# Kernel optimization log

Measured on AMD Instinct MI355X. Metric: run time of the kernel, lower is better.

## Reference

```python
import jax, jax.numpy as jnp
import numpy as np

DIM = 192
NUM_HEADS = 6
WH, WW = 7, 7
N = WH * WW  # 49 tokens per window
C2 = 2 * DIM  # concatenated channel dim = 384
SCALE = (DIM // NUM_HEADS) ** -0.5  # module uses dim//num_heads, not C2//num_heads
NW = 64  # number of windows per image
B_ = 2048  # num_windows * batch


def _relative_position_index():
    ch = np.arange(WH)
    cw = np.arange(WW)
    coords = np.stack(np.meshgrid(ch, cw, indexing='ij')).reshape(2, -1)  # [2, N]
    rel = coords[:, :, None] - coords[:, None, :]  # [2, N, N]
    rel = rel.transpose(1, 2, 0).astype(np.int64)  # [N, N, 2]
    rel[..., 0] += WH - 1
    rel[..., 1] += WW - 1
    rel[..., 0] *= 2 * WW - 1
    return jnp.asarray(rel.sum(-1))  # [N, N]

REL_IDX = _relative_position_index()


def setup_inputs() -> dict:
    key = jax.random.key(0)
    ks = jax.random.split(key, 8)
    x = jax.random.normal(ks[0], (B_, N, DIM), dtype=jnp.float32)
    y = jax.random.normal(ks[1], (B_, N, DIM), dtype=jnp.float32)
    mask = jax.random.normal(ks[2], (NW, N, N), dtype=jnp.float32)
    w_qkv = jax.random.normal(ks[3], (6 * DIM, C2), dtype=jnp.float32) * 0.02
    b_qkv = jnp.zeros((6 * DIM,), dtype=jnp.float32)
    w_proj = jax.random.normal(ks[4], (DIM, C2), dtype=jnp.float32) * 0.02
    b_proj = jnp.zeros((DIM,), dtype=jnp.float32)
    bias_table = jax.random.normal(ks[5], ((2 * WH - 1) * (2 * WW - 1), NUM_HEADS), dtype=jnp.float32) * 0.02
    return {"x": x, "y": y, "mask": mask, "w_qkv": w_qkv, "b_qkv": b_qkv,
            "w_proj": w_proj, "b_proj": b_proj, "bias_table": bias_table}


def reference(x, y, mask, w_qkv, b_qkv, w_proj, b_proj, bias_table):
    Bc = x.shape[0]
    Dh = C2 // NUM_HEADS  # 64
    xy = jnp.concatenate([x, y], axis=2)  # [B_, N, 2*dim]
    qkv = xy @ w_qkv.T + b_qkv  # [B_, N, 6*dim]
    qkv = qkv.reshape(Bc, N, 3, NUM_HEADS, Dh).transpose(2, 0, 3, 1, 4)  # [3, B_, H, N, Dh]
    q, k, v = qkv[0] * SCALE, qkv[1], qkv[2]
    attn = jnp.einsum('bhnd,bhmd->bhnm', q, k)  # [B_, H, N, N]
    rpb = bias_table[REL_IDX]  # [N, N, H]
    attn = attn + rpb.transpose(2, 0, 1)[None]
    nW = mask.shape[0]
    attn = attn.reshape(Bc // nW, nW, NUM_HEADS, N, N) + mask[None, :, None]
    attn = attn.reshape(Bc, NUM_HEADS, N, N)
    attn = jax.nn.softmax(attn, axis=-1)
    out = jnp.einsum('bhnm,bhmd->bhnd', attn, v)  # [B_, H, N, Dh]
    out = out.transpose(0, 2, 1, 3).reshape(Bc, N, C2)
    return out @ w_proj.T + b_proj  # [B_, N, dim]
```

## Files before the change

kernel.cpp:

```cpp
#include <hip/hip_runtime.h>
#include <hip/hip_bf16.h>


typedef __attribute__((ext_vector_type(8))) short short8;
typedef __attribute__((ext_vector_type(4))) float f32x4;

#define SCALE 0.17677669529663687f

#define WQF_OFF    0ul
#define WQF_BYTES  (864ul*1024)
#define WPF_OFF    (WQF_OFF + WQF_BYTES)
#define WPF_BYTES  (144ul*1024)
#define COMB_OFF   (WPF_OFF + WPF_BYTES)
#define COMB_BYTES (64ul*6*4096*4)
#define WS_NEED    (COMB_OFF + COMB_BYTES)

__device__ __forceinline__ unsigned short f2bf(float f){
  unsigned u = __builtin_bit_cast(unsigned, f);
  u = u + 0x7fffu + ((u >> 16) & 1u);
  return (unsigned short)(u >> 16);
}
__device__ __forceinline__ unsigned long long pack4(float4 v){
  return (unsigned long long)f2bf(v.x) | ((unsigned long long)f2bf(v.y) << 16)
       | ((unsigned long long)f2bf(v.z) << 32) | ((unsigned long long)f2bf(v.w) << 48);
}

__device__ __forceinline__ unsigned short cvt1(float x){
  unsigned r;
  asm("v_cvt_pk_bf16_f32 %0, %1, %1" : "=v"(r) : "v"(x));
  return (unsigned short)r;
}
__device__ __forceinline__ uint2 pk4(float a, float b, float c, float d){
  unsigned lo, hi;
  asm("v_cvt_pk_bf16_f32 %0, %1, %2" : "=v"(lo) : "v"(a), "v"(b));
  asm("v_cvt_pk_bf16_f32 %0, %1, %2" : "=v"(hi) : "v"(c), "v"(d));
  return make_uint2(lo, hi);
}

__global__ void k0_wfrag(const float* __restrict__ wq_f, const float* __restrict__ wp_f,
                         unsigned short* __restrict__ wqf, unsigned short* __restrict__ wpf){
  int t = blockIdx.x*256 + threadIdx.x;
  int fragidx = t >> 6, l = t & 63;
  const float* src; unsigned short* dst;
  float sc = 1.0f;
  if (fragidx < 864){
    int h = fragidx/144, rem = fragidx - h*144;
    int ct = rem/12, kt = rem - ct*12;
    int row = (ct>>2)*384 + h*64 + (ct&3)*16 + (l&15);
    src = wq_f + (long)row*384 + kt*32 + (l>>4)*8;
    dst = wqf + (long)fragidx*512 + l*8;
    if (ct < 4) sc = SCALE;
  } else {
    int fid = fragidx - 864;
    int ct = fid/12, kt = fid - ct*12;
    int row = ct*16 + (l&15);
    src = wp_f + (long)row*384 + kt*32 + (l>>4)*8;
    dst = wpf + (long)fid*512 + l*8;
  }
  short8 v;
  #pragma unroll
  for (int e = 0; e < 8; ++e) v[e] = (short)f2bf(src[e] * sc);
  *(short8*)dst = v;
}

__global__ void prep_comb(const float* __restrict__ mask, const float* __restrict__ btab,
                          float* __restrict__ comb){
  int idx = blockIdx.x * 256 + threadIdx.x;
  int j = idx & 63, i = (idx >> 6) & 63, rest = idx >> 12;
  int h = rest % 6, w = rest / 6;
  float v;
  if (i < 49 && j < 49){
    int di = i / 7 - j / 7 + 6;
    int dj = i % 7 - j % 7 + 6;
    v = btab[(di * 13 + dj) * 6 + h] + mask[(w * 49 + i) * 49 + j];
  } else {
    v = (j >= 49) ? -1e30f : 0.0f;
  }
  comb[idx] = v;
}

__device__ __forceinline__ int swz(int r, int b){ return b ^ ((r & 7) << 4); }
__device__ __forceinline__ int a_q (int r, int c){ return 49152 + swz(r, r*128 + c*2); }
__device__ __forceinline__ int a_k (int r, int c){ return 57344 + swz(r, r*128 + c*2); }
__device__ __forceinline__ int a_vt(int r, int c){ return 65536 + swz(r, r*128 + c*2); }
#define OBUF 73728

__global__ __launch_bounds__(256, 2)
void k_fused(const float* __restrict__ x, const float* __restrict__ y,
             const unsigned short* __restrict__ wqf, const unsigned short* __restrict__ wpf,
             const float* __restrict__ bqkv, const float* __restrict__ bproj,
             const float* __restrict__ comb, float* __restrict__ out){
  __shared__ __align__(16) unsigned char smem[81920];
  const int win = blockIdx.x;
  const int tid = threadIdx.x, w = tid>>6, l = tid&63, l15 = l&15, lg = l>>4;

  #pragma unroll
  for (int i = 0; i < 12; ++i){
    int f  = w*12 + i;
    int kt = f >> 2, mt = f & 3;
    int row = mt*16 + l15;
    int c   = kt*32 + lg*8;
    uint4 vv = make_uint4(0,0,0,0);
    if (row < 49){
      const float* src = (c < 192) ? (x + ((long)win*49 + row)*192 + c)
                                   : (y + ((long)win*49 + row)*192 + (c - 192));
      float4 f0 = *(const float4*)src, f1 = *(const float4*)(src + 4);
      uint2 lo = pk4(f0.x, f0.y, f0.z, f0.w);
      uint2 hi = pk4(f1.x, f1.y, f1.z, f1.w);
      vv = make_uint4(lo.x, lo.y, hi.x, hi.y);
    }
    *(uint4*)(smem + f*1024 + l*16) = vv;
  }

  int np[3];
  f32x4 pacc[4][3];
  #pragma unroll
  for (int nt = 0; nt < 3; ++nt){
    np[nt] = w*48 + nt*16 + l15;
    float bv = bproj[np[nt]];
    #pragma unroll
    for (int mt = 0; mt < 4; ++mt)
      #pragma unroll
      for (int j = 0; j < 4; ++j) pacc[mt][nt][j] = bv;
  }

  __syncthreads();

  #pragma unroll 1
  for (int h = 0; h < 6; ++h){
    const float* cb = comb + ((long)((win & 63)*6 + h))*4096 + (w*16 + l15)*64 + lg*4;
    float4 cbv[4];
    #pragma unroll
    for (int nt = 0; nt < 4; ++nt) cbv[nt] = *(const float4*)(cb + nt*16);

    float bias[3];
    #pragma unroll
    for (int nt = 0; nt < 3; ++nt){
      int ct = w*3 + nt, s = ct >> 2;
      bias[nt] = bqkv[s*384 + h*64 + (ct & 3)*16 + l15];
      if (s == 0) bias[nt] *= SCALE;
    }

    const unsigned short* Bb = wqf + ((long)h*12 + w*3)*12*512;
    short8 bB[2][3];
    #pragma unroll
    for (int nt = 0; nt < 3; ++nt)
      bB[0][nt] = *(const short8*)(Bb + (nt*12)*512 + l*8);
    f32x4 acc[4][3];
    #pragma unroll
    for (int mt = 0; mt < 4; ++mt)
      #pragma unroll
      for (int nt = 0; nt < 3; ++nt)
        #pragma unroll
        for (int j = 0; j < 4; ++j) acc[mt][nt][j] = bias[nt];

    #pragma unroll
    for (int kt = 0; kt < 12; ++kt){
      const int cur = kt & 1, nxt = cur ^ 1;
      if (kt < 11){
        #pragma unroll
        for (int nt = 0; nt < 3; ++nt)
          bB[nxt][nt] = *(const short8*)(Bb + (nt*12 + kt+1)*512 + l*8);
      }
      short8 aA[4];
      #pragma unroll
      for (int mt = 0; mt < 4; ++mt)
        aA[mt] = *(const short8*)(smem + (kt*4 + mt)*1024 + l*16);
      __builtin_amdgcn_s_setprio(1);
      #pragma unroll
      for (int nt = 0; nt < 3; ++nt){
        #pragma unroll
        for (int mt = 0; mt < 4; ++mt)
          acc[mt][nt] = __builtin_amdgcn_mfma_f32_16x16x32_bf16(aA[mt], bB[cur][nt], acc[mt][nt], 0, 0, 0);
      }
      __builtin_amdgcn_s_setprio(0);
    }

    #pragma unroll
    for (int nt = 0; nt < 3; ++nt){
      int ct = w*3 + nt, s = ct >> 2, d16 = (ct & 3) * 16;
      if (s == 2){
        #pragma unroll
        for (int mt = 0; mt < 4; ++mt){
          uint2 p = pk4(acc[mt][nt][0], acc[mt][nt][1], acc[mt][nt][2], acc[mt][nt][3]);
          *(uint2*)(smem + a_vt(d16 + l15, mt*16 + lg*4)) = p;
        }
      } else {
        #pragma unroll
        for (int mt = 0; mt < 4; ++mt){
          #pragma unroll
          for (int j = 0; j < 4; ++j){
            int row = mt*16 + lg*4 + j;
            int addr = (s == 0) ? a_q(row, d16 + l15) : a_k(row, d16 + l15);
            *(unsigned short*)(smem + addr) = cvt1(acc[mt][nt][j]);
          }
        }
      }
    }
    __syncthreads();

    short8 bq[2];
    #pragma unroll
    for (int ks = 0; ks < 2; ++ks)
      bq[ks] = *(const short8*)(smem + a_q(w*16 + l15, ks*32 + lg*8));
    f32x4 st[4] = {};
    __builtin_amdgcn_s_setprio(1);
    #pragma unroll
    for (int ks = 0; ks < 2; ++ks){
      #pragma unroll
      for (int nt = 0; nt < 4; ++nt){
        short8 ak = *(const short8*)(smem + a_k(nt*16 + l15, ks*32 + lg*8));
        st[nt] = __builtin_amdgcn_mfma_f32_16x16x32_bf16(ak, bq[ks], st[nt], 0, 0, 0);
      }
    }
    __builtin_amdgcn_s_setprio(0);
    #pragma unroll
    for (int nt = 0; nt < 4; ++nt){
      st[nt][0] += cbv[nt].x; st[nt][1] += cbv[nt].y;
      st[nt][2] += cbv[nt].z; st[nt][3] += cbv[nt].w;
    }
    float mx;
    {
      float m0 = fmaxf(fmaxf(st[0][0], st[0][1]), fmaxf(st[0][2], st[0][3]));
      float m1 = fmaxf(fmaxf(st[1][0], st[1][1]), fmaxf(st[1][2], st[1][3]));
      float m2 = fmaxf(fmaxf(st[2][0], st[2][1]), fmaxf(st[2][2], st[2][3]));
      float m3 = fmaxf(fmaxf(st[3][0], st[3][1]), fmaxf(st[3][2], st[3][3]));
      mx = fmaxf(fmaxf(m0, m1), fmaxf(m2, m3));
    }
    mx = fmaxf(mx, __shfl_xor(mx, 16));
    mx = fmaxf(mx, __shfl_xor(mx, 32));
    float ssum = 0.f;
    #pragma unroll
    for (int nt = 0; nt < 4; ++nt){
      #pragma unroll
      for (int j = 0; j < 4; ++j){
        float e = __expf(st[nt][j] - mx);
        st[nt][j] = e; ssum += e;
      }
    }
    ssum += __shfl_xor(ssum, 16);
    ssum += __shfl_xor(ssum, 32);
    const float inv = 1.0f / ssum;

    #pragma unroll
    for (int nt = 0; nt < 4; ++nt){
      uint2 p = pk4(st[nt][0]*inv, st[nt][1]*inv, st[nt][2]*inv, st[nt][3]*inv);
      *(uint2*)(smem + a_q(w*16 + l15, nt*16 + lg*4)) = p;
    }

    short8 ap[2];
    #pragma unroll
    for (int ks = 0; ks < 2; ++ks)
      ap[ks] = *(const short8*)(smem + a_q(w*16 + l15, ks*32 + lg*8));
    f32x4 oacc[4] = {};
    __builtin_amdgcn_s_setprio(1);
    #pragma unroll
    for (int ks = 0; ks < 2; ++ks){
      #pragma unroll
      for (int nt = 0; nt < 4; ++nt){
        short8 bv = *(const short8*)(smem + a_vt(nt*16 + l15, ks*32 + lg*8));
        oacc[nt] = __builtin_amdgcn_mfma_f32_16x16x32_bf16(ap[ks], bv, oacc[nt], 0, 0, 0);
      }
    }
    __builtin_amdgcn_s_setprio(0);
    #pragma unroll
    for (int nt = 0; nt < 4; ++nt){
      int frag  = (nt >> 1)*4 + w;
      int chunk0 = (lg*4) + ((nt & 1)*2 + (l15 >> 3))*16;
      #pragma unroll
      for (int j = 0; j < 4; ++j){
        int addr = OBUF + frag*1024 + (chunk0 + j)*16 + (l15 & 7)*2;
        *(unsigned short*)(smem + addr) = cvt1(oacc[nt][j]);
      }
    }
    __syncthreads();

    #pragma unroll
    for (int ks = 0; ks < 2; ++ks){
      short8 aO[4];
      #pragma unroll
      for (int mt = 0; mt < 4; ++mt)
        aO[mt] = *(const short8*)(smem + OBUF + (ks*4 + mt)*1024 + l*16);
      __builtin_amdgcn_s_setprio(1);
      #pragma unroll
      for (int nt = 0; nt < 3; ++nt){
        short8 bb = *(const short8*)(wpf + ((long)(w*3 + nt)*12 + h*2 + ks)*512 + l*8);
        #pragma unroll
        for (int mt = 0; mt < 4; ++mt)
          pacc[mt][nt] = __builtin_amdgcn_mfma_f32_16x16x32_bf16(aO[mt], bb, pacc[mt][nt], 0, 0, 0);
      }
      __builtin_amdgcn_s_setprio(0);
    }
  }

  #pragma unroll
  for (int mt = 0; mt < 4; ++mt){
    #pragma unroll
    for (int j = 0; j < 4; ++j){
      int row = mt*16 + lg*4 + j;
      if (row < 49){
        float* o = out + ((long)win*49 + row)*192;
        #pragma unroll
        for (int nt = 0; nt < 3; ++nt)
          o[np[nt]] = pacc[mt][nt][j];
      }
    }
  }
}

#define FB_WQ_ELEMS (1152*384)
#define FB_WP_ELEMS (192*384)
#define FB_WP_OFF   (FB_WQ_ELEMS*2)
#define FB_COMB_OFF (FB_WP_OFF + FB_WP_ELEMS*2)

__global__ void prep_weights_fb(const float* __restrict__ wq_f, const float* __restrict__ wp_f,
                                unsigned short* __restrict__ wq, unsigned short* __restrict__ wp){
  int gid = blockIdx.x * 256 + threadIdx.x;
  if (gid < FB_WQ_ELEMS) wq[gid] = f2bf(wq_f[gid]);
  else { int g = gid - FB_WQ_ELEMS; if (g < FB_WP_ELEMS) wp[g] = f2bf(wp_f[g]); }
}
__device__ __forceinline__ int fb_xy(int r, int c){ return 0      + swz(r, r*768 + c*2); }
__device__ __forceinline__ int fb_q (int r, int c){ return 49152  + swz(r, r*128 + c*2); }
__device__ __forceinline__ int fb_k (int r, int c){ return 57344  + swz(r, r*128 + c*2); }
__device__ __forceinline__ int fb_vt(int r, int c){ return 65536  + swz(r, r*128 + c*2); }
__device__ __forceinline__ int fb_p (int r, int c){ return 73728  + swz(r, r*128 + c*2); }

__global__ __launch_bounds__(256, 2)
void fused_attn_fb(const float* __restrict__ x, const float* __restrict__ y,
                   const float* __restrict__ bqkv, const float* __restrict__ bproj,
                   const unsigned short* __restrict__ wq, const unsigned short* __restrict__ wp,
                   const float* __restrict__ comb, float* __restrict__ out){
  __shared__ __align__(16) unsigned char smem[81920];
  const int b = blockIdx.x, tid = threadIdx.x;
  const int w = tid>>6, l = tid&63, l15 = l&15, lg = l>>4;
  {
    const float4* x4 = (const float4*)x + b * 2352;
    const float4* y4 = (const float4*)y + b * 2352;
    for (int idx = tid; idx < 2352; idx += 256){
      int r = idx / 48, c4 = (idx % 48) * 4;
      float4 vx = x4[idx], vy = y4[idx];
      *(unsigned long long*)(smem + fb_xy(r, c4))       = pack4(vx);
      *(unsigned long long*)(smem + fb_xy(r, 192 + c4)) = pack4(vy);
    }
    for (int idx = tid; idx < 1440; idx += 256){
      int r = 49 + idx / 96, c4 = (idx % 96) * 4;
      *(unsigned long long*)(smem + fb_xy(r, c4)) = 0ull;
    }
  }
  __syncthreads();
  const float* cbB = comb + (long)(b & 63) * (6 * 4096);
  f32x4 pacc[4][3] = {};
  int np[3]; float bp[3];
  #pragma unroll
  for (int nt = 0; nt < 3; ++nt){ np[nt] = w*48 + nt*16 + l15; bp[nt] = bproj[np[nt]]; }
  #pragma unroll 1
  for (int h = 0; h < 6; ++h){
    f32x4 acc[4][3] = {};
    int wrow[3]; float bias[3];
    #pragma unroll
    for (int nt = 0; nt < 3; ++nt){
      int n = np[nt];
      wrow[nt] = (n >> 6) * 384 + h * 64 + (n & 63);
      bias[nt] = bqkv[wrow[nt]];
    }
    #pragma unroll 4
    for (int kt = 0; kt < 12; ++kt){
      int k0 = kt * 32;
      short8 a[4];
      #pragma unroll
      for (int mt = 0; mt < 4; ++mt)
        a[mt] = *(const short8*)(smem + fb_xy(mt*16 + l15, k0 + lg*8));
      #pragma unroll
      for (int nt = 0; nt < 3; ++nt){
        short8 bb = *(const short8*)(wq + (long)wrow[nt]*384 + k0 + lg*8);
        #pragma unroll
        for (int mt = 0; mt < 4; ++mt)
          acc[mt][nt] = __builtin_amdgcn_mfma_f32_16x16x32_bf16(a[mt], bb, acc[mt][nt], 0, 0, 0);
      }
    }
    #pragma unroll
    for (int nt = 0; nt < 3; ++nt){
      int n = np[nt], s = n >> 6, d = n & 63;
      #pragma unroll
      for (int mt = 0; mt < 4; ++mt){
        #pragma unroll
        for (int j = 0; j < 4; ++j){
          int row = mt*16 + lg*4 + j;
          float v = acc[mt][nt][j] + bias[nt];
          if (s == 0) v *= SCALE;
          int addr = (s==0) ? fb_q(row,d) : (s==1) ? fb_k(row,d) : fb_vt(d,row);
          *(unsigned short*)(smem + addr) = f2bf(v);
        }
      }
    }
    __syncthreads();
    short8 aq[2];
    #pragma unroll
    for (int ks = 0; ks < 2; ++ks)
      aq[ks] = *(const short8*)(smem + fb_q(w*16 + l15, ks*32 + lg*8));
    f32x4 sacc[4] = {};
    #pragma unroll
    for (int ks = 0; ks < 2; ++ks)
      #pragma unroll
      for (int nt = 0; nt < 4; ++nt){
        short8 bk = *(const short8*)(smem + fb_k(nt*16 + l15, ks*32 + lg*8));
        sacc[nt] = __builtin_amdgcn_mfma_f32_16x16x32_bf16(aq[ks], bk, sacc[nt], 0, 0, 0);
      }
    const float* cb = cbB + h * 4096;
    float rs[4];
    #pragma unroll
    for (int j = 0; j < 4; ++j){
      int r = w*16 + lg*4 + j;
      #pragma unroll
      for (int nt = 0; nt < 4; ++nt) sacc[nt][j] += cb[r*64 + nt*16 + l15];
      float m = fmaxf(fmaxf(sacc[0][j], sacc[1][j]), fmaxf(sacc[2][j], sacc[3][j]));
      #pragma unroll
      for (int dlt = 1; dlt < 16; dlt <<= 1) m = fmaxf(m, __shfl_xor(m, dlt));
      float ssum = 0.f;
      #pragma unroll
      for (int nt = 0; nt < 4; ++nt){
        float e = __expf(sacc[nt][j] - m);
        sacc[nt][j] = e; ssum += e;
      }
      #pragma unroll
      for (int dlt = 1; dlt < 16; dlt <<= 1) ssum += __shfl_xor(ssum, dlt);
      rs[j] = ssum;
      #pragma unroll
      for (int nt = 0; nt < 4; ++nt)
        *(unsigned short*)(smem + fb_p(r, nt*16 + l15)) = f2bf(sacc[nt][j]);
    }
    short8 ap[2];
    #pragma unroll
    for (int ks = 0; ks < 2; ++ks)
      ap[ks] = *(const short8*)(smem + fb_p(w*16 + l15, ks*32 + lg*8));
    f32x4 oacc[4] = {};
    #pragma unroll
    for (int ks = 0; ks < 2; ++ks)
      #pragma unroll
      for (int nt = 0; nt < 4; ++nt){
        short8 bv = *(const short8*)(smem + fb_vt(nt*16 + l15, ks*32 + lg*8));
        oacc[nt] = __builtin_amdgcn_mfma_f32_16x16x32_bf16(ap[ks], bv, oacc[nt], 0, 0, 0);
      }
    float inv[4];
    #pragma unroll
    for (int j = 0; j < 4; ++j) inv[j] = 1.0f / rs[j];
    #pragma unroll
    for (int nt = 0; nt < 4; ++nt)
      #pragma unroll
      for (int j = 0; j < 4; ++j){
        int row = w*16 + lg*4 + j;
        *(unsigned short*)(smem + fb_p(row, nt*16 + l15)) = f2bf(oacc[nt][j] * inv[j]);
      }
    __syncthreads();
    #pragma unroll
    for (int ks = 0; ks < 2; ++ks){
      short8 ao8[4];
      #pragma unroll
      for (int mt = 0; mt < 4; ++mt)
        ao8[mt] = *(const short8*)(smem + fb_p(mt*16 + l15, ks*32 + lg*8));
      #pragma unroll
      for (int nt = 0; nt < 3; ++nt){
        short8 bb = *(const short8*)(wp + (long)np[nt]*384 + h*64 + ks*32 + lg*8);
        #pragma unroll
        for (int mt = 0; mt < 4; ++mt)
          pacc[mt][nt] = __builtin_amdgcn_mfma_f32_16x16x32_bf16(ao8[mt], bb, pacc[mt][nt], 0, 0, 0);
      }
    }
  }
  #pragma unroll
  for (int mt = 0; mt < 4; ++mt)
    #pragma unroll
    for (int j = 0; j < 4; ++j){
      int row = mt*16 + lg*4 + j;
      if (row < 49){
        float* o = out + ((long)b*49 + row)*192;
        #pragma unroll
        for (int nt = 0; nt < 3; ++nt)
          o[np[nt]] = pacc[mt][nt][j] + bp[nt];
      }
    }
}

extern "C" void kernel_launch(void* const* d_in, const int* in_sizes, int n_in,
                              void* d_out, int out_size, void* d_ws, size_t ws_size,
                              hipStream_t stream){
  (void)in_sizes; (void)n_in; (void)out_size;
  const float* x     = (const float*)d_in[0];
  const float* y     = (const float*)d_in[1];
  const float* mask  = (const float*)d_in[2];
  const float* wq_f  = (const float*)d_in[3];
  const float* bqkv  = (const float*)d_in[4];
  const float* wp_f  = (const float*)d_in[5];
  const float* bproj = (const float*)d_in[6];
  const float* btab  = (const float*)d_in[7];
  float* out = (float*)d_out;

  if (ws_size >= WS_NEED){
    unsigned short* wqf = (unsigned short*)((char*)d_ws + WQF_OFF);
    unsigned short* wpf = (unsigned short*)((char*)d_ws + WPF_OFF);
    float*          cmb = (float*)((char*)d_ws + COMB_OFF);
    hipLaunchKernelGGL(k0_wfrag,  dim3(252),  dim3(256), 0, stream, wq_f, wp_f, wqf, wpf);
    hipLaunchKernelGGL(prep_comb, dim3(6144), dim3(256), 0, stream, mask, btab, cmb);
    hipLaunchKernelGGL(k_fused,   dim3(2048), dim3(256), 0, stream,
                       x, y, wqf, wpf, bqkv, bproj, cmb, out);
  } else {
    unsigned short* wq  = (unsigned short*)d_ws;
    unsigned short* wp  = (unsigned short*)((char*)d_ws + FB_WP_OFF);
    float*          cmb = (float*)((char*)d_ws + FB_COMB_OFF);
    hipLaunchKernelGGL(prep_weights_fb, dim3(2016), dim3(256), 0, stream, wq_f, wp_f, wq, wp);
    hipLaunchKernelGGL(prep_comb,       dim3(6144), dim3(256), 0, stream, mask, btab, cmb);
    hipLaunchKernelGGL(fused_attn_fb,   dim3(2048), dim3(256), 0, stream,
                       x, y, bqkv, bproj, wq, wp, cmb, out);
  }
}
```

Measured before the change: 220.6 us.

## Merge prep kernels into one launch, hoist proj weight loads, unroll head loop

Combines the weight-fragment conversion and the bias/mask precompute into a single k_prep launch, removing one kernel launch and its gap. Inside the fused kernel, the projection-weight fragments for each head are loaded into registers before the output-scatter barrier so the global-load latency overlaps other work. The head loop is unrolled by two to give the scheduler more freedom. Each change raises register pressure, which could reduce occupancy under the two-blocks-per-CU launch bound.

Result: slower. 270.7 us (+22.7%).

```diff
diff --git a/kernel.cpp b/kernel.cpp
--- a/kernel.cpp
+++ b/kernel.cpp
@@ -37,46 +37,47 @@
   return make_uint2(lo, hi);
 }
 
-__global__ void k0_wfrag(const float* __restrict__ wq_f, const float* __restrict__ wp_f,
-                         unsigned short* __restrict__ wqf, unsigned short* __restrict__ wpf){
-  int t = blockIdx.x*256 + threadIdx.x;
-  int fragidx = t >> 6, l = t & 63;
-  const float* src; unsigned short* dst;
-  float sc = 1.0f;
-  if (fragidx < 864){
-    int h = fragidx/144, rem = fragidx - h*144;
-    int ct = rem/12, kt = rem - ct*12;
-    int row = (ct>>2)*384 + h*64 + (ct&3)*16 + (l&15);
-    src = wq_f + (long)row*384 + kt*32 + (l>>4)*8;
-    dst = wqf + (long)fragidx*512 + l*8;
-    if (ct < 4) sc = SCALE;
+__global__ void k_prep(const float* __restrict__ wq_f, const float* __restrict__ wp_f,
+                       const float* __restrict__ mask, const float* __restrict__ btab,
+                       unsigned short* __restrict__ wqf, unsigned short* __restrict__ wpf,
+                       float* __restrict__ comb){
+  if (blockIdx.x < 252){
+    int t = blockIdx.x*256 + threadIdx.x;
+    int fragidx = t >> 6, l = t & 63;
+    const float* src; unsigned short* dst;
+    float sc = 1.0f;
+    if (fragidx < 864){
+      int h = fragidx/144, rem = fragidx - h*144;
+      int ct = rem/12, kt = rem - ct*12;
+      int row = (ct>>2)*384 + h*64 + (ct&3)*16 + (l&15);
+      src = wq_f + (long)row*384 + kt*32 + (l>>4)*8;
+      dst = wqf + (long)fragidx*512 + l*8;
+      if (ct < 4) sc = SCALE;
+    } else {
+      int fid = fragidx - 864;
+      int ct = fid/12, kt = fid - ct*12;
+      int row = ct*16 + (l&15);
+      src = wp_f + (long)row*384 + kt*32 + (l>>4)*8;
+      dst = wpf + (long)fid*512 + l*8;
+    }
+    short8 v;
+    #pragma unroll
+    for (int e = 0; e < 8; ++e) v[e] = (short)f2bf(src[e] * sc);
+    *(short8*)dst = v;
   } else {
-    int fid = fragidx - 864;
-    int ct = fid/12, kt = fid - ct*12;
-    int row = ct*16 + (l&15);
-    src = wp_f + (long)row*384 + kt*32 + (l>>4)*8;
-    dst = wpf + (long)fid*512 + l*8;
-  }
-  short8 v;
-  #pragma unroll
-  for (int e = 0; e < 8; ++e) v[e] = (short)f2bf(src[e] * sc);
-  *(short8*)dst = v;
-}
-
-__global__ void prep_comb(const float* __restrict__ mask, const float* __restrict__ btab,
-                          float* __restrict__ comb){
-  int idx = blockIdx.x * 256 + threadIdx.x;
-  int j = idx & 63, i = (idx >> 6) & 63, rest = idx >> 12;
-  int h = rest % 6, w = rest / 6;
-  float v;
-  if (i < 49 && j < 49){
-    int di = i / 7 - j / 7 + 6;
-    int dj = i % 7 - j % 7 + 6;
-    v = btab[(di * 13 + dj) * 6 + h] + mask[(w * 49 + i) * 49 + j];
-  } else {
-    v = (j >= 49) ? -1e30f : 0.0f;
-  }
-  comb[idx] = v;
+    int idx = (blockIdx.x - 252)*256 + threadIdx.x;
+    int j = idx & 63, i = (idx >> 6) & 63, rest = idx >> 12;
+    int h = rest % 6, w = rest / 6;
+    float v;
+    if (i < 49 && j < 49){
+      int di = i / 7 - j / 7 + 6;
+      int dj = i % 7 - j % 7 + 6;
+      v = btab[(di * 13 + dj) * 6 + h] + mask[(w * 49 + i) * 49 + j];
+    } else {
+      v = (j >= 49) ? -1e30f : 0.0f;
+    }
+    comb[idx] = v;
+  }
 }
 
 __device__ __forceinline__ int swz(int r, int b){ return b ^ ((r & 7) << 4); }
@@ -126,7 +127,7 @@
 
   __syncthreads();
 
-  #pragma unroll 1
+  #pragma unroll 2
   for (int h = 0; h < 6; ++h){
     const float* cb = comb + ((long)((win & 63)*6 + h))*4096 + (w*16 + l15)*64 + lg*4;
     float4 cbv[4];
@@ -263,6 +264,14 @@
       }
     }
     __builtin_amdgcn_s_setprio(0);
+
+    short8 pb[2][3];
+    #pragma unroll
+    for (int ks = 0; ks < 2; ++ks)
+      #pragma unroll
+      for (int nt = 0; nt < 3; ++nt)
+        pb[ks][nt] = *(const short8*)(wpf + ((long)(w*3 + nt)*12 + h*2 + ks)*512 + l*8);
+
     #pragma unroll
     for (int nt = 0; nt < 4; ++nt){
       int frag  = (nt >> 1)*4 + w;
@@ -284,10 +293,9 @@
       __builtin_amdgcn_s_setprio(1);
       #pragma unroll
       for (int nt = 0; nt < 3; ++nt){
-        short8 bb = *(const short8*)(wpf + ((long)(w*3 + nt)*12 + h*2 + ks)*512 + l*8);
         #pragma unroll
         for (int mt = 0; mt < 4; ++mt)
-          pacc[mt][nt] = __builtin_amdgcn_mfma_f32_16x16x32_bf16(aO[mt], bb, pacc[mt][nt], 0, 0, 0);
+          pacc[mt][nt] = __builtin_amdgcn_mfma_f32_16x16x32_bf16(aO[mt], pb[ks][nt], pacc[mt][nt], 0, 0, 0);
       }
       __builtin_amdgcn_s_setprio(0);
     }
@@ -318,6 +326,21 @@
   int gid = blockIdx.x * 256 + threadIdx.x;
   if (gid < FB_WQ_ELEMS) wq[gid] = f2bf(wq_f[gid]);
   else { int g = gid - FB_WQ_ELEMS; if (g < FB_WP_ELEMS) wp[g] = f2bf(wp_f[g]); }
+}
+__global__ void prep_comb_fb(const float* __restrict__ mask, const float* __restrict__ btab,
+                             float* __restrict__ comb){
+  int idx = blockIdx.x * 256 + threadIdx.x;
+  int j = idx & 63, i = (idx >> 6) & 63, rest = idx >> 12;
+  int h = rest % 6, w = rest / 6;
+  float v;
+  if (i < 49 && j < 49){
+    int di = i / 7 - j / 7 + 6;
+    int dj = i % 7 - j % 7 + 6;
+    v = btab[(di * 13 + dj) * 6 + h] + mask[(w * 49 + i) * 49 + j];
+  } else {
+    v = (j >= 49) ? -1e30f : 0.0f;
+  }
+  comb[idx] = v;
 }
 __device__ __forceinline__ int fb_xy(int r, int c){ return 0      + swz(r, r*768 + c*2); }
 __device__ __forceinline__ int fb_q (int r, int c){ return 49152  + swz(r, r*128 + c*2); }
@@ -499,16 +522,16 @@
     unsigned short* wqf = (unsigned short*)((char*)d_ws + WQF_OFF);
     unsigned short* wpf = (unsigned short*)((char*)d_ws + WPF_OFF);
     float*          cmb = (float*)((char*)d_ws + COMB_OFF);
-    hipLaunchKernelGGL(k0_wfrag,  dim3(252),  dim3(256), 0, stream, wq_f, wp_f, wqf, wpf);
-    hipLaunchKernelGGL(prep_comb, dim3(6144), dim3(256), 0, stream, mask, btab, cmb);
-    hipLaunchKernelGGL(k_fused,   dim3(2048), dim3(256), 0, stream,
+    hipLaunchKernelGGL(k_prep,  dim3(6396), dim3(256), 0, stream,
+                       wq_f, wp_f, mask, btab, wqf, wpf, cmb);
+    hipLaunchKernelGGL(k_fused, dim3(2048), dim3(256), 0, stream,
                        x, y, wqf, wpf, bqkv, bproj, cmb, out);
   } else {
     unsigned short* wq  = (unsigned short*)d_ws;
     unsigned short* wp  = (unsigned short*)((char*)d_ws + FB_WP_OFF);
     float*          cmb = (float*)((char*)d_ws + FB_COMB_OFF);
     hipLaunchKernelGGL(prep_weights_fb, dim3(2016), dim3(256), 0, stream, wq_f, wp_f, wq, wp);
-    hipLaunchKernelGGL(prep_comb,       dim3(6144), dim3(256), 0, stream, mask, btab, cmb);
+    hipLaunchKernelGGL(prep_comb_fb,    dim3(6144), dim3(256), 0, stream, mask, btab, cmb);
     hipLaunchKernelGGL(fused_attn_fb,   dim3(2048), dim3(256), 0, stream,
                        x, y, bqkv, bproj, wq, wp, cmb, out);
   }
```
